# Optimization experiments

Measured on AMD Instinct MI355X. Metric: run time of the kernel, lower is better.

## Reference

```python
import jax, jax.numpy as jnp
import numpy as np

M, T = 256, 1024
PADDED_N = 2 * T  # max(T,T)*2 per original code


def _pairwise_max_cross_corr(zis, zjs):
    # Center along time axis
    f1 = zis - jnp.mean(zis, axis=-1, keepdims=True)   # (M, T)
    f2 = zjs - jnp.mean(zjs, axis=-1, keepdims=True)   # (M, T)
    # Zero-pad to 2T and take real FFTs once per row (vectorizes the python loop)
    F1 = jnp.fft.rfft(f1, n=PADDED_N, axis=-1)         # (M, F) complex
    F2 = jnp.fft.rfft(f2, n=PADDED_N, axis=-1)         # (M, F) complex
    # Pairwise cross-spectrum: X[i, j] = F1[i] * conj(F2[j])
    X = F1[:, None, :] * jnp.conj(F2)[None, :, :]      # (M, M, F)
    # torch.std is unbiased (ddof=1)
    s1 = jnp.std(f1, axis=-1, ddof=1)                  # (M,)
    s2 = jnp.std(f2, axis=-1, ddof=1)                  # (M,)
    power = s1[:, None] * s2[None, :]                  # (M, M)
    power = jnp.where(power == 0, jnp.ones_like(power), power)
    cc = jnp.fft.irfft(X / power[:, :, None], n=PADDED_N, axis=-1) / (T - 1)  # (M, M, 2T)
    return jnp.max(cc, axis=-1)                        # (M, M)


def setup_inputs() -> dict:
    key = jax.random.key(0)
    k1, k2, k3 = jax.random.split(key, 3)
    zis = jax.random.normal(k1, (M, T), dtype=jnp.float32)
    zjs = jax.random.normal(k2, (M, T), dtype=jnp.float32)
    speeds = jax.random.randint(k3, (M,), 0, M, dtype=jnp.int64)
    return {"zis": zis, "zjs": zjs, "speeds": speeds}


def reference(zis, zjs, speeds):
    dist = _pairwise_max_cross_corr(zis, zjs)          # logits (M, M)
    # CrossEntropyLoss(reduction='sum')
    logp = jax.nn.log_softmax(dist, axis=-1)
    loss = -jnp.sum(logp[jnp.arange(dist.shape[0]), speeds])
    return loss
```

## Files before the change

kernel.cpp:

```cpp
#include <hip/hip_runtime.h>
#include <hip/hip_bf16.h>

#define M_ROWS 256
#define T_LEN  1024
#define NLAG   2048
#define CPYB   656
#define CPCH   39
#define NCOPY4 32
#define GPZW4  260

typedef __attribute__((ext_vector_type(4)))  unsigned int u32x4;
typedef __attribute__((ext_vector_type(8)))  int          i32x8;
typedef __attribute__((ext_vector_type(16))) float        f32x16;

static __device__ __forceinline__ unsigned short f2bf(float f) {
  unsigned int u = __builtin_bit_cast(unsigned int, f);
  u += 0x7FFFu + ((u >> 16) & 1u);
  return (unsigned short)(u >> 16);
}

static __device__ __forceinline__ unsigned int fp4enc(float c) {
  float a = fabsf(c);
  unsigned int code = (unsigned int)(a >= 0.25f) + (unsigned int)(a >= 0.75f) +
                      (unsigned int)(a >= 1.25f) + (unsigned int)(a >= 1.75f) +
                      (unsigned int)(a >= 2.5f)  + (unsigned int)(a >= 3.5f) +
                      (unsigned int)(a >= 5.0f);
  return code | ((__builtin_bit_cast(unsigned int, c) >> 28) & 8u);
}

__global__ __launch_bounds__(256) void prep_kernel(
    const float* __restrict__ zis, const float* __restrict__ zjs,
    unsigned int* __restrict__ f1p4, unsigned int* __restrict__ gpz4,
    float* __restrict__ s1, float* __restrict__ s2, float* __restrict__ out) {
  int r = blockIdx.x;
  const float* src = (r < M_ROWS) ? (zis + r * T_LEN) : (zjs + (r - M_ROWS) * T_LEN);
  int t = threadIdx.x;
  if (r == 0 && t == 0) out[0] = 0.0f;
  float4 v = reinterpret_cast<const float4*>(src)[t];
  float ls = v.x + v.y + v.z + v.w;
  for (int m = 1; m <= 32; m <<= 1) ls += __shfl_xor(ls, m, 64);
  __shared__ float red[4];
  __shared__ float red2[4];
  if ((t & 63) == 0) red[t >> 6] = ls;
  __syncthreads();
  float mean = (red[0] + red[1] + red[2] + red[3]) * (1.0f / 1024.0f);
  float c0 = v.x - mean, c1 = v.y - mean, c2 = v.z - mean, c3 = v.w - mean;
  float ss = c0 * c0 + c1 * c1 + c2 * c2 + c3 * c3;
  for (int m = 1; m <= 32; m <<= 1) ss += __shfl_xor(ss, m, 64);
  if ((t & 63) == 0) red2[t >> 6] = ss;
  __syncthreads();
  float sd = sqrtf((red2[0] + red2[1] + red2[2] + red2[3]) * (1.0f / 1023.0f));

  unsigned int h16 = fp4enc(c0) | (fp4enc(c1) << 4) | (fp4enc(c2) << 8) | (fp4enc(c3) << 12);
  unsigned int other = (unsigned int)__shfl_xor((int)h16, 1, 64);
  unsigned int word = h16 | (other << 16);

  if (r < M_ROWS) {
    if (t == 0) s1[r] = sd;
    if (!(t & 1)) {
      int ks = t >> 4, l5 = (t >> 3) & 1, w = (t & 7) >> 1;
      f1p4[((ks * 2 + l5) * 256 + r) * 4 + w] = word;
    }
  } else {
    int j = r - M_ROWS;
    if (t == 0) s2[j] = sd;
    if (!(t & 1)) gpz4[j * GPZW4 + (t >> 1)] = word;
    if (t >= 128) gpz4[j * GPZW4 + t] = 0u;
    if (!(t & 1) && (t >> 1) < 4) gpz4[j * GPZW4 + 256 + (t >> 1)] = word;
  }
}

#define LOADF_P(F0, F1)                                   \
  {                                                       \
    ((u32x4*)&(F0))[0] = *(const u32x4*)(fp);             \
    ((u32x4*)&(F1))[0] = *(const u32x4*)(fp + 128);       \
    fp += 2048;                                           \
  }

#define LDG4A(GA, GB, GC, GD)                                       \
  {                                                                 \
    ((u32x4*)&(GA))[0] = *(const u32x4*)(ldsB + gb + 48);           \
    ((u32x4*)&(GB))[0] = *(const u32x4*)(ldsB + gb + 32);           \
    ((u32x4*)&(GC))[0] = *(const u32x4*)(ldsB + gb + 16);           \
    ((u32x4*)&(GD))[0] = *(const u32x4*)(ldsB + gb);                \
    gb += 32;                                                       \
  }

#define STEP8(GA, GB, GC, GD, F0, F1)                                                        \
  {                                                                                          \
    z00 = __builtin_amdgcn_mfma_scale_f32_32x32x64_f8f6f4(GA, F0, z00, 4, 4, 0, 127, 0, 127); \
    z10 = __builtin_amdgcn_mfma_scale_f32_32x32x64_f8f6f4(GA, F1, z10, 4, 4, 0, 127, 0, 127); \
    z01 = __builtin_amdgcn_mfma_scale_f32_32x32x64_f8f6f4(GB, F0, z01, 4, 4, 0, 127, 0, 127); \
    z11 = __builtin_amdgcn_mfma_scale_f32_32x32x64_f8f6f4(GB, F1, z11, 4, 4, 0, 127, 0, 127); \
    z02 = __builtin_amdgcn_mfma_scale_f32_32x32x64_f8f6f4(GC, F0, z02, 4, 4, 0, 127, 0, 127); \
    z12 = __builtin_amdgcn_mfma_scale_f32_32x32x64_f8f6f4(GC, F1, z12, 4, 4, 0, 127, 0, 127); \
    z03 = __builtin_amdgcn_mfma_scale_f32_32x32x64_f8f6f4(GD, F0, z03, 4, 4, 0, 127, 0, 127); \
    z13 = __builtin_amdgcn_mfma_scale_f32_32x32x64_f8f6f4(GD, F1, z13, 4, 4, 0, 127, 0, 127); \
  }

__global__ __launch_bounds__(256, 2) void corr_kernel(
    const unsigned int* __restrict__ f1p4,
    const unsigned int* __restrict__ gpz4,
    unsigned short* __restrict__ part) {
  __shared__ __align__(16) unsigned char ldsB[NCOPY4 * CPYB];
  __shared__ float red[2][256];

  int wg = blockIdx.x;
  int j = wg & 255;
  int bp = wg >> 8;

  int tid = threadIdx.x;
  int lane = tid & 63;
  int rw = tid >> 6;
  int l5 = lane >> 5;
  int l31 = lane & 31;

  {
    const unsigned int* gj = gpz4 + j * GPZW4;
#pragma unroll
    for (int m = 0; m < 5; ++m) {
      int ch = m * 256 + tid;
      if (ch < NCOPY4 * CPCH) {
        int cp = ch / CPCH;
        int cc = ch - cp * CPCH;
        int s = 32 * cc - 96 - cp;
        int m0 = s + ((s < 0) ? 2048 : 0);
        int wb = m0 >> 3;
        int sh = (m0 & 7) << 2;
        unsigned int w0 = gj[wb], w1 = gj[wb + 1], w2 = gj[wb + 2],
                     w3 = gj[wb + 3], w4 = gj[wb + 4];
        u32x4 o;
        if (sh) {
          o[0] = (w0 >> sh) | (w1 << (32 - sh));
          o[1] = (w1 >> sh) | (w2 << (32 - sh));
          o[2] = (w2 >> sh) | (w3 << (32 - sh));
          o[3] = (w3 >> sh) | (w4 << (32 - sh));
        } else {
          o[0] = w0; o[1] = w1; o[2] = w2; o[3] = w3;
        }
        *reinterpret_cast<u32x4*>(ldsB + cp * CPYB + cc * 16) = o;
      }
    }
  }
  __syncthreads();

  const unsigned int* fbase = f1p4 + l5 * 1024 + ((rw * 64 + l31) << 2);
  int gb_lane = l31 * CPYB + 16 * l5;

#pragma unroll 1
  for (int pc = 0; pc < 2; ++pc) {
    int blk = pc ? (bp + 8) : bp;
    int kA = pc ? 0 : (bp << 1);
    int kB = pc ? ((bp << 1) + 2) : 16;

    int gb = gb_lane + (pc ? (512 - 64 * bp) : 0);
    const unsigned int* fp = fbase + kA * 2048;

    f32x16 z00, z01, z02, z03, z10, z11, z12, z13;
#pragma unroll
    for (int q = 0; q < 16; ++q) {
      z00[q] = 0.f; z01[q] = 0.f; z02[q] = 0.f; z03[q] = 0.f;
      z10[q] = 0.f; z11[q] = 0.f; z12[q] = 0.f; z13[q] = 0.f;
    }

    i32x8 X0 = {0,0,0,0,0,0,0,0}, X1 = {0,0,0,0,0,0,0,0};
    i32x8 X2 = {0,0,0,0,0,0,0,0}, X3 = {0,0,0,0,0,0,0,0};
    i32x8 Y0 = {0,0,0,0,0,0,0,0}, Y1 = {0,0,0,0,0,0,0,0};
    i32x8 Y2 = {0,0,0,0,0,0,0,0}, Y3 = {0,0,0,0,0,0,0,0};
    i32x8 Fx0 = {0,0,0,0,0,0,0,0}, Fx1 = {0,0,0,0,0,0,0,0};
    i32x8 Fy0 = {0,0,0,0,0,0,0,0}, Fy1 = {0,0,0,0,0,0,0,0};

    LDG4A(X0, X1, X2, X3);
    LOADF_P(Fx0, Fx1);
    int ks = kA;
#pragma unroll 1
    for (; ks + 2 < kB; ks += 2) {
      LDG4A(Y0, Y1, Y2, Y3);
      LOADF_P(Fy0, Fy1);
      STEP8(X0, X1, X2, X3, Fx0, Fx1);
      LDG4A(X0, X1, X2, X3);
      LOADF_P(Fx0, Fx1);
      STEP8(Y0, Y1, Y2, Y3, Fy0, Fy1);
    }
    LDG4A(Y0, Y1, Y2, Y3);
    LOADF_P(Fy0, Fy1);
    STEP8(X0, X1, X2, X3, Fx0, Fx1);
    STEP8(Y0, Y1, Y2, Y3, Fy0, Fy1);

    float a0 = fmaxf(fmaxf(z00[0], z01[0]), fmaxf(z02[0], z03[0]));
    float a1 = fmaxf(fmaxf(z10[0], z11[0]), fmaxf(z12[0], z13[0]));
#pragma unroll
    for (int q = 1; q < 16; ++q) {
      a0 = fmaxf(a0, fmaxf(fmaxf(z00[q], z01[q]), fmaxf(z02[q], z03[q])));
      a1 = fmaxf(a1, fmaxf(fmaxf(z10[q], z11[q]), fmaxf(z12[q], z13[q])));
    }
    a0 = fmaxf(a0, __shfl_xor(a0, 32, 64));
    a1 = fmaxf(a1, __shfl_xor(a1, 32, 64));
    if (l5 == 0) {
      red[pc][rw * 64 + l31] = a0;
      red[pc][rw * 64 + 32 + l31] = a1;
    }
    __syncthreads();
    part[(tid * 16 + blk) * 256 + j] = f2bf(red[pc][tid]);
  }
}

__global__ __launch_bounds__(256) void loss_kernel(
    const unsigned short* __restrict__ part, const float* __restrict__ s1,
    const float* __restrict__ s2, const int* __restrict__ speeds,
    float* __restrict__ out) {
  int i = blockIdx.x;
  int jt = threadIdx.x;
  unsigned short um = part[(i * 16 + 0) * 256 + jt];
  float m = __builtin_bit_cast(float, ((unsigned int)um) << 16);
#pragma unroll
  for (int b = 1; b < 16; ++b) {
    unsigned short ub = part[(i * 16 + b) * 256 + jt];
    m = fmaxf(m, __builtin_bit_cast(float, ((unsigned int)ub) << 16));
  }
  float p = s1[i] * s2[jt];
  p = (p == 0.0f) ? 1.0f : p;
  float d = m / (p * 1023.0f);

  float t = d;
  for (int mk = 1; mk <= 32; mk <<= 1) t = fmaxf(t, __shfl_xor(t, mk, 64));
  __shared__ float wmax[4], wsum[4], sel;
  if ((jt & 63) == 0) wmax[jt >> 6] = t;
  if (jt == speeds[i]) sel = d;
  __syncthreads();
  float rmax = fmaxf(fmaxf(wmax[0], wmax[1]), fmaxf(wmax[2], wmax[3]));
  float e = expf(d - rmax);
  for (int mk = 1; mk <= 32; mk <<= 1) e += __shfl_xor(e, mk, 64);
  if ((jt & 63) == 0) wsum[jt >> 6] = e;
  __syncthreads();
  if (jt == 0) {
    float sum = wsum[0] + wsum[1] + wsum[2] + wsum[3];
    atomicAdd(out, rmax + logf(sum) - sel);
  }
}

extern "C" void kernel_launch(void* const* d_in, const int* in_sizes, int n_in,
                              void* d_out, int out_size, void* d_ws, size_t ws_size,
                              hipStream_t stream) {
  (void)in_sizes; (void)n_in; (void)out_size; (void)ws_size;
  const float* zis = (const float*)d_in[0];
  const float* zjs = (const float*)d_in[1];
  const int* speeds = (const int*)d_in[2];
  float* out = (float*)d_out;

  char* ws = (char*)d_ws;
  unsigned int* f1p4 = (unsigned int*)ws;
  unsigned int* gpz4 = (unsigned int*)(ws + 131072);
  float* s1 = (float*)(ws + 131072 + 266240);
  float* s2 = (float*)(ws + 131072 + 266240 + 1024);
  unsigned short* part = (unsigned short*)(ws + 131072 + 266240 + 2048);

  prep_kernel<<<512, 256, 0, stream>>>(zis, zjs, f1p4, gpz4, s1, s2, out);
  corr_kernel<<<2048, 256, 0, stream>>>(f1p4, gpz4, part);
  loss_kernel<<<256, 256, 0, stream>>>(part, s1, s2, speeds, out);
}
```

Measured before the change: 53.14 us.

## Split lag tiles across twice as many workgroups with fewer accumulators each

Each corr_kernel workgroup now computes half of the lag columns it covered before: two of four 32-lag MFMA tiles, selected by a new half index. The grid doubles to 4096 workgroups and the launch bound goes from 2 to 3 waves per SIMD, which cuts accumulator and operand registers to allow higher occupancy. The cost is that every workgroup repeats the full LDS staging of the shifted g row and reloads the F operands, doubling that traffic. The partial-max buffer doubles to 32 slices, so loss_kernel reads twice as many partials.

```diff
diff --git a/kernel.cpp b/kernel.cpp
--- a/kernel.cpp
+++ b/kernel.cpp
@@ -77,28 +77,22 @@
     fp += 2048;                                           \
   }
 
-#define LDG4A(GA, GB, GC, GD)                                       \
+#define LDG2A(GA, GB)                                               \
   {                                                                 \
-    ((u32x4*)&(GA))[0] = *(const u32x4*)(ldsB + gb + 48);           \
-    ((u32x4*)&(GB))[0] = *(const u32x4*)(ldsB + gb + 32);           \
-    ((u32x4*)&(GC))[0] = *(const u32x4*)(ldsB + gb + 16);           \
-    ((u32x4*)&(GD))[0] = *(const u32x4*)(ldsB + gb);                \
+    ((u32x4*)&(GA))[0] = *(const u32x4*)(ldsB + gb + 16);           \
+    ((u32x4*)&(GB))[0] = *(const u32x4*)(ldsB + gb);                \
     gb += 32;                                                       \
   }
 
-#define STEP8(GA, GB, GC, GD, F0, F1)                                                        \
+#define STEP4(GA, GB, F0, F1)                                                                \
   {                                                                                          \
     z00 = __builtin_amdgcn_mfma_scale_f32_32x32x64_f8f6f4(GA, F0, z00, 4, 4, 0, 127, 0, 127); \
     z10 = __builtin_amdgcn_mfma_scale_f32_32x32x64_f8f6f4(GA, F1, z10, 4, 4, 0, 127, 0, 127); \
     z01 = __builtin_amdgcn_mfma_scale_f32_32x32x64_f8f6f4(GB, F0, z01, 4, 4, 0, 127, 0, 127); \
     z11 = __builtin_amdgcn_mfma_scale_f32_32x32x64_f8f6f4(GB, F1, z11, 4, 4, 0, 127, 0, 127); \
-    z02 = __builtin_amdgcn_mfma_scale_f32_32x32x64_f8f6f4(GC, F0, z02, 4, 4, 0, 127, 0, 127); \
-    z12 = __builtin_amdgcn_mfma_scale_f32_32x32x64_f8f6f4(GC, F1, z12, 4, 4, 0, 127, 0, 127); \
-    z03 = __builtin_amdgcn_mfma_scale_f32_32x32x64_f8f6f4(GD, F0, z03, 4, 4, 0, 127, 0, 127); \
-    z13 = __builtin_amdgcn_mfma_scale_f32_32x32x64_f8f6f4(GD, F1, z13, 4, 4, 0, 127, 0, 127); \
-  }
-
-__global__ __launch_bounds__(256, 2) void corr_kernel(
+  }
+
+__global__ __launch_bounds__(256, 3) void corr_kernel(
     const unsigned int* __restrict__ f1p4,
     const unsigned int* __restrict__ gpz4,
     unsigned short* __restrict__ part) {
@@ -107,7 +101,9 @@
 
   int wg = blockIdx.x;
   int j = wg & 255;
-  int bp = wg >> 8;
+  int bh = wg >> 8;
+  int bp = bh >> 1;
+  int lh = bh & 1;
 
   int tid = threadIdx.x;
   int lane = tid & 63;
@@ -145,7 +141,7 @@
   __syncthreads();
 
   const unsigned int* fbase = f1p4 + l5 * 1024 + ((rw * 64 + l31) << 2);
-  int gb_lane = l31 * CPYB + 16 * l5;
+  int gb_lane = l31 * CPYB + 16 * l5 - 32 * lh + 32;
 
 #pragma unroll 1
   for (int pc = 0; pc < 2; ++pc) {
@@ -156,43 +152,38 @@
     int gb = gb_lane + (pc ? (512 - 64 * bp) : 0);
     const unsigned int* fp = fbase + kA * 2048;
 
-    f32x16 z00, z01, z02, z03, z10, z11, z12, z13;
-#pragma unroll
-    for (int q = 0; q < 16; ++q) {
-      z00[q] = 0.f; z01[q] = 0.f; z02[q] = 0.f; z03[q] = 0.f;
-      z10[q] = 0.f; z11[q] = 0.f; z12[q] = 0.f; z13[q] = 0.f;
-    }
-
-    i32x8 X0 = {0,0,0,0,0,0,0,0}, X1 = {0,0,0,0,0,0,0,0};
-    i32x8 X2 = {0,0,0,0,0,0,0,0}, X3 = {0,0,0,0,0,0,0,0};
-    i32x8 Y0 = {0,0,0,0,0,0,0,0}, Y1 = {0,0,0,0,0,0,0,0};
-    i32x8 Y2 = {0,0,0,0,0,0,0,0}, Y3 = {0,0,0,0,0,0,0,0};
+    f32x16 z00, z01, z10, z11;
+#pragma unroll
+    for (int q = 0; q < 16; ++q) { z00[q] = 0.f; z01[q] = 0.f; z10[q] = 0.f; z11[q] = 0.f; }
+
+    i32x8 XA = {0,0,0,0,0,0,0,0}, XB = {0,0,0,0,0,0,0,0};
+    i32x8 YA = {0,0,0,0,0,0,0,0}, YB = {0,0,0,0,0,0,0,0};
     i32x8 Fx0 = {0,0,0,0,0,0,0,0}, Fx1 = {0,0,0,0,0,0,0,0};
     i32x8 Fy0 = {0,0,0,0,0,0,0,0}, Fy1 = {0,0,0,0,0,0,0,0};
 
-    LDG4A(X0, X1, X2, X3);
+    LDG2A(XA, XB);
     LOADF_P(Fx0, Fx1);
     int ks = kA;
 #pragma unroll 1
     for (; ks + 2 < kB; ks += 2) {
-      LDG4A(Y0, Y1, Y2, Y3);
+      LDG2A(YA, YB);
       LOADF_P(Fy0, Fy1);
-      STEP8(X0, X1, X2, X3, Fx0, Fx1);
-      LDG4A(X0, X1, X2, X3);
+      STEP4(XA, XB, Fx0, Fx1);
+      LDG2A(XA, XB);
       LOADF_P(Fx0, Fx1);
-      STEP8(Y0, Y1, Y2, Y3, Fy0, Fy1);
-    }
-    LDG4A(Y0, Y1, Y2, Y3);
+      STEP4(YA, YB, Fy0, Fy1);
+    }
+    LDG2A(YA, YB);
     LOADF_P(Fy0, Fy1);
-    STEP8(X0, X1, X2, X3, Fx0, Fx1);
-    STEP8(Y0, Y1, Y2, Y3, Fy0, Fy1);
-
-    float a0 = fmaxf(fmaxf(z00[0], z01[0]), fmaxf(z02[0], z03[0]));
-    float a1 = fmaxf(fmaxf(z10[0], z11[0]), fmaxf(z12[0], z13[0]));
+    STEP4(XA, XB, Fx0, Fx1);
+    STEP4(YA, YB, Fy0, Fy1);
+
+    float a0 = fmaxf(z00[0], z01[0]);
+    float a1 = fmaxf(z10[0], z11[0]);
 #pragma unroll
     for (int q = 1; q < 16; ++q) {
-      a0 = fmaxf(a0, fmaxf(fmaxf(z00[q], z01[q]), fmaxf(z02[q], z03[q])));
-      a1 = fmaxf(a1, fmaxf(fmaxf(z10[q], z11[q]), fmaxf(z12[q], z13[q])));
+      a0 = fmaxf(a0, fmaxf(z00[q], z01[q]));
+      a1 = fmaxf(a1, fmaxf(z10[q], z11[q]));
     }
     a0 = fmaxf(a0, __shfl_xor(a0, 32, 64));
     a1 = fmaxf(a1, __shfl_xor(a1, 32, 64));
@@ -201,7 +192,7 @@
       red[pc][rw * 64 + 32 + l31] = a1;
     }
     __syncthreads();
-    part[(tid * 16 + blk) * 256 + j] = f2bf(red[pc][tid]);
+    part[(tid * 32 + blk * 2 + lh) * 256 + j] = f2bf(red[pc][tid]);
   }
 }
 
@@ -211,11 +202,11 @@
     float* __restrict__ out) {
   int i = blockIdx.x;
   int jt = threadIdx.x;
-  unsigned short um = part[(i * 16 + 0) * 256 + jt];
+  unsigned short um = part[(i * 32 + 0) * 256 + jt];
   float m = __builtin_bit_cast(float, ((unsigned int)um) << 16);
 #pragma unroll
-  for (int b = 1; b < 16; ++b) {
-    unsigned short ub = part[(i * 16 + b) * 256 + jt];
+  for (int b = 1; b < 32; ++b) {
+    unsigned short ub = part[(i * 32 + b) * 256 + jt];
     m = fmaxf(m, __builtin_bit_cast(float, ((unsigned int)ub) << 16));
   }
   float p = s1[i] * s2[jt];
@@ -256,6 +247,6 @@
   unsigned short* part = (unsigned short*)(ws + 131072 + 266240 + 2048);
 
   prep_kernel<<<512, 256, 0, stream>>>(zis, zjs, f1p4, gpz4, s1, s2, out);
-  corr_kernel<<<2048, 256, 0, stream>>>(f1p4, gpz4, part);
+  corr_kernel<<<4096, 256, 0, stream>>>(f1p4, gpz4, part);
   loss_kernel<<<256, 256, 0, stream>>>(part, s1, s2, speeds, out);
 }
```

New measurement: 62.76 us. 18.1% more time.
